# Kernel tuning notes

Measured on AMD Instinct MI355X. Metric: run time of the kernel, lower is better.

## Reference

```python
import jax, jax.numpy as jnp
import numpy as np

B, Q, P, K, E, H = 2, 2500, 2500, 2500, 256, 8
D = E // H
FF = 2 * E
EPS = 1e-5


def layernorm(x, g, b):
    mu = jnp.mean(x, axis=-1, keepdims=True)
    var = jnp.var(x, axis=-1, keepdims=True)
    return (x - mu) * jax.lax.rsqrt(var + EPS) * g + b


def mha(q_in, k_in, v_in, wq, wk, wv, scale):
    n, ql = q_in.shape[0], q_in.shape[1]
    q = (q_in @ wq).reshape(n, ql, H, D)
    k = (k_in @ wk).reshape(n, k_in.shape[1], H, D)
    v = (v_in @ wv).reshape(n, v_in.shape[1], H, D)
    scores = jnp.einsum('nqhd,nkhd->nhqk', q, k) / scale
    attn = jax.nn.softmax(scores, axis=-1)
    return jnp.einsum('nhqk,nkhd->nqhd', attn, v).reshape(n, ql, E)


def setup_inputs() -> dict:
    key = jax.random.key(0)
    ks = jax.random.split(key, 24)
    s = lambda i, shape, sc=0.02: jax.random.normal(ks[i], shape, dtype=jnp.float32) * sc
    return {
        'prev_seq': jax.random.normal(ks[0], (B, P, E), dtype=jnp.float32),
        'query': jax.random.normal(ks[1], (B, Q, E), dtype=jnp.float32),
        'img_ft': jax.random.normal(ks[2], (B, K, E), dtype=jnp.float32),
        't_wq': s(3, (E, E)), 't_wk': s(4, (E, E)), 't_wv': s(5, (E, E)),
        's_wq': s(6, (E, E)), 's_wk': s(7, (E, E)), 's_wv': s(8, (E, E)),
        's_wo': s(9, (E, E)), 's_bo': jnp.zeros((E,), jnp.float32),
        'n1_g': jnp.ones((E,), jnp.float32), 'n1_b': jnp.zeros((E,), jnp.float32),
        'n2_g': jnp.ones((E,), jnp.float32), 'n2_b': jnp.zeros((E,), jnp.float32),
        'n3_g': jnp.ones((E,), jnp.float32), 'n3_b': jnp.zeros((E,), jnp.float32),
        'ff_w1': s(10, (E, FF)), 'ff_b1': jnp.zeros((FF,), jnp.float32),
        'ff_w2': s(11, (FF, E)), 'ff_b2': jnp.zeros((E,), jnp.float32),
    }


def reference(prev_seq, query, img_ft, t_wq, t_wk, t_wv, s_wq, s_wk, s_wv,
              s_wo, s_bo, n1_g, n1_b, n2_g, n2_b, n3_g, n3_b,
              ff_w1, ff_b1, ff_w2, ff_b2):
    # Temporal self-attention: K/V from prev_seq, scale = sqrt(embed_size)
    attn = mha(query, prev_seq, prev_seq, t_wq, t_wk, t_wv, float(E) ** 0.5)
    x = layernorm(attn + query, n1_g, n1_b)
    # Spatial cross-attention: K/V from img_ft, scale = sqrt(head_dim), with fc_out
    cross = mha(x, img_ft, img_ft, s_wq, s_wk, s_wv, float(D) ** 0.5)
    cross = cross @ s_wo + s_bo
    x = layernorm(cross + x, n2_g, n2_b)
    # FFN: E -> 2E -> ReLU -> E
    ff = jax.nn.relu(x @ ff_w1 + ff_b1) @ ff_w2 + ff_b2
    return layernorm(ff + x, n3_g, n3_b)
```

## Files before the change

kernel.cpp:

```cpp
#include <hip/hip_runtime.h>
#include <hip/hip_bf16.h>
#include <stdint.h>


typedef __bf16 bf16_t;
typedef __bf16 bf16x8 __attribute__((ext_vector_type(8)));
typedef __bf16 bf16x4 __attribute__((ext_vector_type(4)));
typedef float  f32x4  __attribute__((ext_vector_type(4)));
typedef float  f32x16 __attribute__((ext_vector_type(16)));
typedef uint32_t u32;
typedef uint32_t u32x4 __attribute__((ext_vector_type(4)));

#define NB   2
#define SEQ  2500
#define EMB  256
#define NH   8
#define HD   32
#define MTOT (NB*SEQ)
#define KVSPLIT 5
#define SPLITLEN 500
#define NTILE 16

static __device__ __forceinline__ f32x4 mfma16(bf16x8 a, bf16x8 b, f32x4 c) {
  return __builtin_amdgcn_mfma_f32_16x16x32_bf16(a, b, c, 0, 0, 0);
}
static __device__ __forceinline__ f32x16 mfma32(bf16x8 a, bf16x8 b, f32x16 c) {
  return __builtin_amdgcn_mfma_f32_32x32x16_bf16(a, b, c, 0, 0, 0);
}
static __device__ __forceinline__ u32 pack2(float a, float b) {
  union { __bf16 h; unsigned short s; } x, y;
  x.h = (__bf16)a; y.h = (__bf16)b;
  return (u32)x.s | ((u32)y.s << 16);
}

__global__ __launch_bounds__(256) void prep_kernel(
    const float* s0, const float* s1, const float* s2, const float* s3,
    const float* s4, const float* s5, const float* s6, const float* s7,
    const float* s8, bf16_t* wt,
    const float* aq, const float* ap, const float* ai,
    bf16_t* dq, bf16_t* dp, bf16_t* di)
{
  int b = blockIdx.x;
  if (b < 176) {
    const float* src; int R, C, tl; size_t doff;
    if (b < 112) {
      int mi = b >> 4; tl = b & 15; R = 256; C = 256; doff = (size_t)mi * 65536;
      switch (mi) {
        case 0: src = s0; break; case 1: src = s1; break; case 2: src = s2; break;
        case 3: src = s3; break; case 4: src = s4; break; case 5: src = s5; break;
        default: src = s6;
      }
    } else if (b < 144) { tl = b - 112; R = 256; C = 512; doff = 458752; src = s7; }
    else                { tl = b - 144; R = 512; C = 256; doff = 589824; src = s8; }
    const int tpr = C >> 6;
    const int tr = tl / tpr, tc = tl % tpr;
    bf16_t* dst = wt + doff;
    #pragma unroll
    for (int i = 0; i < 16; ++i) {
      int lin = i * 256 + threadIdx.x;
      int lr = lin >> 6, lc = lin & 63;
      int rr = tr * 64 + lr, cc = tc * 64 + lc;
      dst[(size_t)cc * R + rr] = (__bf16)src[(size_t)rr * C + cc];
    }
    return;
  }
  int idx = b - 176;
  int t = idx / 313, r = idx % 313;
  const float* src = (t == 0) ? aq : (t == 1) ? ap : ai;
  bf16_t* dst = (t == 0) ? dq : (t == 1) ? dp : di;
  #pragma unroll
  for (int k = 0; k < 4; ++k) {
    int i = r * 1024 + k * 256 + threadIdx.x;
    if (i < 320000) {
      float4 v = ((const float4*)src)[i];
      bf16x4 o;
      o[0] = (__bf16)v.x; o[1] = (__bf16)v.y; o[2] = (__bf16)v.z; o[3] = (__bf16)v.w;
      ((bf16x4*)dst)[i] = o;
    }
  }
}

static __device__ __forceinline__ void gemm_body(
    const bf16_t* __restrict__ A, const bf16_t* __restrict__ Wt,
    const float* __restrict__ bias, bf16_t* __restrict__ Cout,
    int M, int N, int K, int relu, float cscale, int bx, int by)
{
  const int tid = threadIdx.x;
  const int lane = tid & 63, wid = tid >> 6;
  const int l15 = lane & 15, g = lane >> 4;
  const int mbase = bx * 64 + wid * 16;
  const int nbase = by * 64;

  int arow = mbase + l15; if (arow > M - 1) arow = M - 1;
  const bf16_t* ap = A + (size_t)arow * K + g * 8;
  const bf16_t* bp = Wt + (size_t)(nbase + l15) * K + g * 8;

  f32x4 acc[4];
  #pragma unroll
  for (int j = 0; j < 4; ++j) acc[j] = (f32x4){0.f,0.f,0.f,0.f};

  for (int kk = 0; kk < K; kk += 32) {
    bf16x8 a = *(const bf16x8*)(ap + kk);
    #pragma unroll
    for (int ct = 0; ct < 4; ++ct) {
      bf16x8 bfr = *(const bf16x8*)(bp + (size_t)ct * 16 * K + kk);
      acc[ct] = mfma16(a, bfr, acc[ct]);
    }
  }
  #pragma unroll
  for (int ct = 0; ct < 4; ++ct) {
    const int col = nbase + ct * 16 + l15;
    const float bv = bias ? bias[col] : 0.f;
    #pragma unroll
    for (int r = 0; r < 4; ++r) {
      const int row = mbase + g * 4 + r;
      if (row < M) {
        float v = acc[ct][r] * cscale + bv;
        if (relu) v = fmaxf(v, 0.f);
        Cout[(size_t)row * N + col] = (bf16_t)v;
      }
    }
  }
}

__global__ __launch_bounds__(256) void gemm_kernel(
    const bf16_t* __restrict__ A, const bf16_t* __restrict__ Wt,
    const float* __restrict__ bias, bf16_t* __restrict__ Cout,
    int M, int N, int K, int relu)
{
  gemm_body(A, Wt, bias, Cout, M, N, K, relu, 1.f, blockIdx.x, blockIdx.y);
}

__global__ __launch_bounds__(256) void proj3_kernel(
    const bf16_t* A0, const bf16_t* W0, bf16_t* C0,
    const bf16_t* A1, const bf16_t* W1, bf16_t* C1,
    const bf16_t* A2, const bf16_t* W2, bf16_t* C2, float qsc)
{
  const bf16_t* A = (blockIdx.z == 0) ? A0 : (blockIdx.z == 1) ? A1 : A2;
  const bf16_t* W = (blockIdx.z == 0) ? W0 : (blockIdx.z == 1) ? W1 : W2;
  bf16_t* C = (blockIdx.z == 0) ? C0 : (blockIdx.z == 1) ? C1 : C2;
  const float cs = (blockIdx.z == 0) ? qsc : 1.f;
  gemm_body(A, W, nullptr, C, MTOT, 256, 256, 0, cs, blockIdx.x, blockIdx.y);
}

__global__ __launch_bounds__(256, 4) void attn_part_kernel(
    const bf16_t* __restrict__ Qm, const bf16_t* __restrict__ Km,
    const bf16_t* __restrict__ Vm, bf16_t* __restrict__ Op,
    float* __restrict__ Lp)
{
  __shared__ bf16_t Vt[2][32][40];

  const int tid = threadIdx.x;
  const int lane = tid & 63, wid = tid >> 6;
  const int q32 = lane & 31, hi = lane >> 5;

  const int n = blockIdx.x;
  const int vid = (n & 7) * 200 + (n >> 3);
  const int grp = vid / 20;
  const int sub = vid - grp * 20;
  const int bh = grp / 5;
  const int split = grp - bh * 5;

  const size_t qoff = (size_t)(bh >> 3) * SEQ * EMB + (bh & 7) * HD;
  const int kv_begin = split * SPLITLEN;
  const int kv_end = kv_begin + SPLITLEN;

  const int qbase = sub * 128 + wid * 32;
  const int qr = min(qbase + q32, SEQ - 1);
  const bf16x8 qfa = *(const bf16x8*)(Qm + qoff + (size_t)qr * EMB + hi * 8);
  const bf16x8 qfb = *(const bf16x8*)(Qm + qoff + (size_t)qr * EMB + 16 + hi * 8);

  f32x16 acc = {};
  float lsum = 0.f;

  const int skv = tid >> 3;
  const int sd0 = (tid & 7) << 2;
  const int scc = (skv + ((sd0 >> 3) << 3)) & 31;

  const bf16_t* kp = Km + qoff + (size_t)(kv_begin + q32) * EMB + hi * 8;
  const bf16_t* vp = Vm + qoff + (size_t)(kv_begin + skv) * EMB + sd0;

  bf16x4 vreg = *(const bf16x4*)vp;
  vp += 32 * EMB;
  bf16x8 ka = *(const bf16x8*)kp;
  bf16x8 kb = *(const bf16x8*)(kp + 16);
  kp += 32 * EMB;

#define ATTN_TILE(T, MASKED, PREFETCH)                                         \
  {                                                                            \
    const int buf = (T) & 1;                                                   \
    _Pragma("unroll")                                                          \
    for (int j = 0; j < 4; ++j) Vt[buf][sd0 + j][scc] = vreg[j];               \
    bf16x4 vnext; bf16x8 kan, kbn;                                             \
    if (PREFETCH) {                                                            \
      vnext = *(const bf16x4*)vp;                                              \
      vp += 32 * EMB;                                                          \
      kan = *(const bf16x8*)kp;                                                \
      kbn = *(const bf16x8*)(kp + 16);                                         \
      kp += 32 * EMB;                                                          \
    }                                                                          \
    __syncthreads();                                                           \
    f32x16 s = {};                                                             \
    s = mfma32(ka, qfa, s);                                                    \
    s = mfma32(kb, qfb, s);                                                    \
    float p[16];                                                               \
    _Pragma("unroll")                                                          \
    for (int r = 0; r < 16; ++r) p[r] = __builtin_amdgcn_exp2f(s[r]);          \
    if (MASKED) {                                                              \
      const int kv0m = kv_begin + ((T) << 5);                                  \
      _Pragma("unroll")                                                        \
      for (int r = 0; r < 16; ++r) {                                           \
        const int kvg = kv0m + (r & 3) + ((r >> 2) << 3) + hi * 4;             \
        if (kvg >= kv_end) p[r] = 0.f;                                         \
      }                                                                        \
    }                                                                          \
    float ps = 0.f;                                                            \
    _Pragma("unroll")                                                          \
    for (int r = 0; r < 16; ++r) ps += p[r];                                   \
    lsum += ps;                                                                \
    u32 w0 = pack2(p[0], p[1]),   w1 = pack2(p[2], p[3]);                      \
    u32 w2 = pack2(p[4], p[5]),   w3 = pack2(p[6], p[7]);                      \
    u32 w4 = pack2(p[8], p[9]),   w5 = pack2(p[10], p[11]);                    \
    u32 w6 = pack2(p[12], p[13]), w7 = pack2(p[14], p[15]);                    \
    asm("v_permlane32_swap_b32 %0, %1" : "+v"(w0), "+v"(w2));                  \
    asm("v_permlane32_swap_b32 %0, %1" : "+v"(w1), "+v"(w3));                  \
    asm("v_permlane32_swap_b32 %0, %1" : "+v"(w4), "+v"(w6));                  \
    asm("v_permlane32_swap_b32 %0, %1" : "+v"(w5), "+v"(w7));                  \
    u32x4 f1, f2;                                                              \
    f1.x = w0; f1.y = w1; f1.z = w2; f1.w = w3;                                \
    f2.x = w4; f2.y = w5; f2.z = w6; f2.w = w7;                                \
    bf16x8 vf1 = *(const bf16x8*)&Vt[buf][q32][(((hi + (q32 >> 3)) & 3) << 3)];\
    bf16x8 vf2 = *(const bf16x8*)&Vt[buf][q32][(((2 + hi + (q32 >> 3)) & 3) << 3)]; \
    acc = mfma32(*(bf16x8*)&f1, vf1, acc);                                     \
    acc = mfma32(*(bf16x8*)&f2, vf2, acc);                                     \
    if (PREFETCH) { ka = kan; kb = kbn; vreg = vnext; }                        \
  }

  #pragma unroll 5
  for (int t = 0; t < NTILE - 1; ++t) ATTN_TILE(t, 0, 1)
  ATTN_TILE(NTILE - 1, 1, 0)
#undef ATTN_TILE

  lsum += __shfl_xor(lsum, 32);
  const size_t pbase = ((size_t)split * 16 + bh) * SEQ;
  #pragma unroll
  for (int r = 0; r < 16; ++r) {
    const int q = qbase + (r & 3) + ((r >> 2) << 3) + hi * 4;
    if (q < SEQ) Op[(pbase + q) * 32 + q32] = (bf16_t)acc[r];
  }
  if (lane < 32) {
    const int q = qbase + lane;
    if (q < SEQ) Lp[pbase + q] = lsum;
  }
}

__global__ __launch_bounds__(256) void merge_kernel(
    const bf16_t* __restrict__ Op, const float* __restrict__ Lp,
    const bf16_t* __restrict__ resid, const float* __restrict__ gw,
    const float* __restrict__ bw, bf16_t* __restrict__ out, int doLN)
{
  const int lane = threadIdx.x & 63, wid = threadIdx.x >> 6;
  const int row = blockIdx.x * 4 + wid;
  const int b = row / SEQ, q = row - b * SEQ;
  const int h = lane >> 3, dl = (lane & 7) * 4;
  const int bh = b * 8 + h;

  float L = 0.f;
  float acc[4] = {0.f, 0.f, 0.f, 0.f};
  #pragma unroll
  for (int s = 0; s < KVSPLIT; ++s) {
    const size_t pb = ((size_t)s * 16 + bh) * SEQ + q;
    L += Lp[pb];
    bf16x4 ov = *(const bf16x4*)(Op + pb * 32 + dl);
    #pragma unroll
    for (int j = 0; j < 4; ++j) acc[j] += (float)ov[j];
  }
  const float invL = 1.f / L;
  const size_t base = (size_t)row * EMB + lane * 4;
  if (!doLN) {
    bf16x4 ov;
    #pragma unroll
    for (int j = 0; j < 4; ++j) ov[j] = (__bf16)(acc[j] * invL);
    *(bf16x4*)(out + base) = ov;
    return;
  }
  bf16x4 rv = *(const bf16x4*)(resid + base);
  float x[4], s = 0.f, sq = 0.f;
  #pragma unroll
  for (int j = 0; j < 4; ++j) {
    x[j] = acc[j] * invL + (float)rv[j];
    s += x[j]; sq += x[j] * x[j];
  }
  #pragma unroll
  for (int m = 1; m < 64; m <<= 1) { s += __shfl_xor(s, m); sq += __shfl_xor(sq, m); }
  const float mean = s * (1.f / EMB);
  const float var = sq * (1.f / EMB) - mean * mean;
  const float rstd = rsqrtf(var + 1e-5f);
  float4 gv = *(const float4*)(gw + lane * 4);
  float4 bv = *(const float4*)(bw + lane * 4);
  bf16x4 ov;
  ov[0] = (__bf16)((x[0] - mean) * rstd * gv.x + bv.x);
  ov[1] = (__bf16)((x[1] - mean) * rstd * gv.y + bv.y);
  ov[2] = (__bf16)((x[2] - mean) * rstd * gv.z + bv.z);
  ov[3] = (__bf16)((x[3] - mean) * rstd * gv.w + bv.w);
  *(bf16x4*)(out + base) = ov;
}

__global__ __launch_bounds__(256) void ln_kernel(
    const bf16_t* __restrict__ A, const bf16_t* __restrict__ Bres,
    const float* __restrict__ gw, const float* __restrict__ bw,
    bf16_t* __restrict__ OutB, float* __restrict__ OutF, int M)
{
  const int lane = threadIdx.x & 63;
  const int wid = threadIdx.x >> 6;
  const int row = blockIdx.x * 4 + wid;
  if (row >= M) return;
  const size_t base = (size_t)row * EMB + lane * 4;
  bf16x4 av = *(const bf16x4*)(A + base);
  bf16x4 bv = *(const bf16x4*)(Bres + base);
  float x[4], s = 0.f, sq = 0.f;
  #pragma unroll
  for (int i = 0; i < 4; ++i) {
    x[i] = (float)av[i] + (float)bv[i];
    s += x[i]; sq += x[i] * x[i];
  }
  #pragma unroll
  for (int m = 1; m < 64; m <<= 1) { s += __shfl_xor(s, m); sq += __shfl_xor(sq, m); }
  const float mean = s * (1.f / EMB);
  const float var = sq * (1.f / EMB) - mean * mean;
  const float rstd = rsqrtf(var + 1e-5f);
  float4 gv = *(const float4*)(gw + lane * 4);
  float4 bev = *(const float4*)(bw + lane * 4);
  float y0 = (x[0] - mean) * rstd * gv.x + bev.x;
  float y1 = (x[1] - mean) * rstd * gv.y + bev.y;
  float y2 = (x[2] - mean) * rstd * gv.z + bev.z;
  float y3 = (x[3] - mean) * rstd * gv.w + bev.w;
  if (OutF) {
    float4 ov = {y0, y1, y2, y3};
    *(float4*)(OutF + base) = ov;
  } else {
    bf16x4 ov;
    ov[0] = (__bf16)y0; ov[1] = (__bf16)y1; ov[2] = (__bf16)y2; ov[3] = (__bf16)y3;
    *(bf16x4*)(OutB + base) = ov;
  }
}

extern "C" void kernel_launch(void* const* d_in, const int* in_sizes, int n_in,
                              void* d_out, int out_size, void* d_ws, size_t ws_size,
                              hipStream_t stream)
{
  (void)in_sizes; (void)n_in; (void)out_size; (void)ws_size;
  const float* prev  = (const float*)d_in[0];
  const float* query = (const float*)d_in[1];
  const float* img   = (const float*)d_in[2];
  const float* t_wq  = (const float*)d_in[3];
  const float* t_wk  = (const float*)d_in[4];
  const float* t_wv  = (const float*)d_in[5];
  const float* s_wq  = (const float*)d_in[6];
  const float* s_wk  = (const float*)d_in[7];
  const float* s_wv  = (const float*)d_in[8];
  const float* s_wo  = (const float*)d_in[9];
  const float* s_bo  = (const float*)d_in[10];
  const float* n1g = (const float*)d_in[11];
  const float* n1b = (const float*)d_in[12];
  const float* n2g = (const float*)d_in[13];
  const float* n2b = (const float*)d_in[14];
  const float* n3g = (const float*)d_in[15];
  const float* n3b = (const float*)d_in[16];
  const float* ffw1 = (const float*)d_in[17];
  const float* ffb1 = (const float*)d_in[18];
  const float* ffw2 = (const float*)d_in[19];
  const float* ffb2 = (const float*)d_in[20];

  bf16_t* ws   = (bf16_t*)d_ws;
  bf16_t* WT   = ws;
  bf16_t* WTF1 = ws + 458752;
  bf16_t* WTF2 = ws + 589824;
  bf16_t* qbf = ws + 720896;
  bf16_t* pbf = qbf + 1280000;
  bf16_t* ibf = pbf + 1280000;
  bf16_t* qb = ibf + 1280000;
  bf16_t* kb = qb + 1280000;
  bf16_t* vb = kb + 1280000;
  bf16_t* ab = vb + 1280000;
  bf16_t* x1 = ab + 1280000;
  bf16_t* cb = x1 + 1280000;
  bf16_t* x2 = cb + 1280000;
  bf16_t* hb = x2 + 1280000;
  bf16_t* fb = hb + 2560000;
  float* outp = (float*)d_out;
  bf16_t* Op = cb;
  float*  Lp = (float*)pbf;

  const float log2e = 1.4426950408889634f;
  const float qscT = log2e * (1.f / 16.f);
  const float qscS = log2e * 0.17677669529663687f;

  dim3 blk(256);
  prep_kernel<<<1115, blk, 0, stream>>>(t_wq, t_wk, t_wv, s_wq, s_wk, s_wv,
                                        s_wo, ffw1, ffw2, ws,
                                        query, prev, img, qbf, pbf, ibf);

  dim3 gP(79, 4, 3), gG256(79, 4), gG512(79, 8);
  proj3_kernel<<<gP, blk, 0, stream>>>(qbf, WT, qb,
                                       pbf, WT + 65536, kb,
                                       pbf, WT + 131072, vb, qscT);
  attn_part_kernel<<<1600, blk, 0, stream>>>(qb, kb, vb, Op, Lp);
  merge_kernel<<<1250, blk, 0, stream>>>(Op, Lp, qbf, n1g, n1b, x1, 1);
  proj3_kernel<<<gP, blk, 0, stream>>>(x1,  WT + 196608, qb,
                                       ibf, WT + 262144, kb,
                                       ibf, WT + 327680, vb, qscS);
  attn_part_kernel<<<1600, blk, 0, stream>>>(qb, kb, vb, Op, Lp);
  merge_kernel<<<1250, blk, 0, stream>>>(Op, Lp, nullptr, nullptr, nullptr, ab, 0);
  gemm_kernel<<<gG256, blk, 0, stream>>>(ab, WT + 393216, s_bo, cb, MTOT, 256, 256, 0);
  ln_kernel<<<1250, blk, 0, stream>>>(cb, x1, n2g, n2b, x2, nullptr, MTOT);
  gemm_kernel<<<gG512, blk, 0, stream>>>(x2, WTF1, ffb1, hb, MTOT, 512, 256, 1);
  gemm_kernel<<<gG256, blk, 0, stream>>>(hb, WTF2, ffb2, fb, MTOT, 256, 512, 0);
  ln_kernel<<<1250, blk, 0, stream>>>(fb, x2, n3g, n3b, nullptr, outp, MTOT);
}
```

Baseline: 197.2 us.

## Process attention KV tiles in pairs with dual accumulators for ILP

Restructures the split-KV attention inner loop to handle two 32-wide KV tiles per iteration, with separate score and output accumulators and interleaved MFMAs. This halves the number of __syncthreads barriers and exposes independent MFMA/exp chains to hide latency. The partial sums are also reduced with a tree instead of a serial chain. In exchange it doubles LDS for V tiles and raises register pressure, which could hurt occupancy under launch_bounds(256,4).

After: 199.5 us. Within noise of the previous version (+1.2%).

```diff
diff --git a/kernel.cpp b/kernel.cpp
--- a/kernel.cpp
+++ b/kernel.cpp
@@ -148,7 +148,7 @@
     const bf16_t* __restrict__ Vm, bf16_t* __restrict__ Op,
     float* __restrict__ Lp)
 {
-  __shared__ bf16_t Vt[2][32][40];
+  __shared__ bf16_t Vt[4][32][40];
 
   const int tid = threadIdx.x;
   const int lane = tid & 63, wid = tid >> 6;
@@ -170,7 +170,7 @@
   const bf16x8 qfa = *(const bf16x8*)(Qm + qoff + (size_t)qr * EMB + hi * 8);
   const bf16x8 qfb = *(const bf16x8*)(Qm + qoff + (size_t)qr * EMB + 16 + hi * 8);
 
-  f32x16 acc = {};
+  f32x16 accA = {}, accB = {};
   float lsum = 0.f;
 
   const int skv = tid >> 3;
@@ -180,73 +180,113 @@
   const bf16_t* kp = Km + qoff + (size_t)(kv_begin + q32) * EMB + hi * 8;
   const bf16_t* vp = Vm + qoff + (size_t)(kv_begin + skv) * EMB + sd0;
 
-  bf16x4 vreg = *(const bf16x4*)vp;
-  vp += 32 * EMB;
-  bf16x8 ka = *(const bf16x8*)kp;
-  bf16x8 kb = *(const bf16x8*)(kp + 16);
-  kp += 32 * EMB;
-
-#define ATTN_TILE(T, MASKED, PREFETCH)                                         \
+  bf16x4 vA = *(const bf16x4*)vp;
+  bf16x4 vB = *(const bf16x4*)(vp + 32 * EMB);
+  bf16x8 kaA = *(const bf16x8*)kp;
+  bf16x8 kbA = *(const bf16x8*)(kp + 16);
+  bf16x8 kaB = *(const bf16x8*)(kp + 32 * EMB);
+  bf16x8 kbB = *(const bf16x8*)(kp + 32 * EMB + 16);
+  kp += 64 * EMB;
+  vp += 64 * EMB;
+
+#define TREE16(dst, p)                                                         \
+    {                                                                          \
+      float t0 = p[0] + p[1],  t1 = p[2] + p[3];                               \
+      float t2 = p[4] + p[5],  t3 = p[6] + p[7];                               \
+      float t4 = p[8] + p[9],  t5 = p[10] + p[11];                             \
+      float t6 = p[12] + p[13], t7 = p[14] + p[15];                            \
+      float u0 = t0 + t1, u1 = t2 + t3, u2 = t4 + t5, u3 = t6 + t7;            \
+      dst = (u0 + u1) + (u2 + u3);                                             \
+    }
+
+#define SOFTPACK(p, f1, f2)                                                    \
+    {                                                                          \
+      u32 w0 = pack2(p[0], p[1]),   w1 = pack2(p[2], p[3]);                    \
+      u32 w2 = pack2(p[4], p[5]),   w3 = pack2(p[6], p[7]);                    \
+      u32 w4 = pack2(p[8], p[9]),   w5 = pack2(p[10], p[11]);                  \
+      u32 w6 = pack2(p[12], p[13]), w7 = pack2(p[14], p[15]);                  \
+      asm("v_permlane32_swap_b32 %0, %1" : "+v"(w0), "+v"(w2));                \
+      asm("v_permlane32_swap_b32 %0, %1" : "+v"(w1), "+v"(w3));                \
+      asm("v_permlane32_swap_b32 %0, %1" : "+v"(w4), "+v"(w6));                \
+      asm("v_permlane32_swap_b32 %0, %1" : "+v"(w5), "+v"(w7));                \
+      f1.x = w0; f1.y = w1; f1.z = w2; f1.w = w3;                              \
+      f2.x = w4; f2.y = w5; f2.z = w6; f2.w = w7;                              \
+    }
+
+#define ATTN_PAIR(P, MASKED, PREFETCH)                                         \
   {                                                                            \
-    const int buf = (T) & 1;                                                   \
+    const int bufA = ((P) & 1) << 1, bufB = bufA + 1;                          \
     _Pragma("unroll")                                                          \
-    for (int j = 0; j < 4; ++j) Vt[buf][sd0 + j][scc] = vreg[j];               \
-    bf16x4 vnext; bf16x8 kan, kbn;                                             \
+    for (int j = 0; j < 4; ++j) {                                              \
+      Vt[bufA][sd0 + j][scc] = vA[j];                                          \
+      Vt[bufB][sd0 + j][scc] = vB[j];                                          \
+    }                                                                          \
+    bf16x4 vAn, vBn; bf16x8 kaAn, kbAn, kaBn, kbBn;                            \
     if (PREFETCH) {                                                            \
-      vnext = *(const bf16x4*)vp;                                              \
-      vp += 32 * EMB;                                                          \
-      kan = *(const bf16x8*)kp;                                                \
-      kbn = *(const bf16x8*)(kp + 16);                                         \
-      kp += 32 * EMB;                                                          \
+      vAn = *(const bf16x4*)vp;                                                \
+      vBn = *(const bf16x4*)(vp + 32 * EMB);                                   \
+      kaAn = *(const bf16x8*)kp;                                               \
+      kbAn = *(const bf16x8*)(kp + 16);                                        \
+      kaBn = *(const bf16x8*)(kp + 32 * EMB);                                  \
+      kbBn = *(const bf16x8*)(kp + 32 * EMB + 16);                             \
+      kp += 64 * EMB; vp += 64 * EMB;                                          \
     }                                                                          \
     __syncthreads();                                                           \
-    f32x16 s = {};                                                             \
-    s = mfma32(ka, qfa, s);                                                    \
-    s = mfma32(kb, qfb, s);                                                    \
-    float p[16];                                                               \
+    f32x16 sA = {}, sB = {};                                                   \
+    sA = mfma32(kaA, qfa, sA);                                                 \
+    sB = mfma32(kaB, qfa, sB);                                                 \
+    sA = mfma32(kbA, qfb, sA);                                                 \
+    sB = mfma32(kbB, qfb, sB);                                                 \
+    float pA[16], pB[16];                                                      \
     _Pragma("unroll")                                                          \
-    for (int r = 0; r < 16; ++r) p[r] = __builtin_amdgcn_exp2f(s[r]);          \
+    for (int r = 0; r < 16; ++r) {                                             \
+      pA[r] = __builtin_amdgcn_exp2f(sA[r]);                                   \
+      pB[r] = __builtin_amdgcn_exp2f(sB[r]);                                   \
+    }                                                                          \
     if (MASKED) {                                                              \
-      const int kv0m = kv_begin + ((T) << 5);                                  \
+      const int kv0m = kv_begin + ((((P) << 1) + 1) << 5);                     \
       _Pragma("unroll")                                                        \
       for (int r = 0; r < 16; ++r) {                                           \
         const int kvg = kv0m + (r & 3) + ((r >> 2) << 3) + hi * 4;             \
-        if (kvg >= kv_end) p[r] = 0.f;                                         \
+        if (kvg >= kv_end) pB[r] = 0.f;                                        \
       }                                                                        \
     }                                                                          \
-    float ps = 0.f;                                                            \
-    _Pragma("unroll")                                                          \
-    for (int r = 0; r < 16; ++r) ps += p[r];                                   \
-    lsum += ps;                                                                \
-    u32 w0 = pack2(p[0], p[1]),   w1 = pack2(p[2], p[3]);                      \
-    u32 w2 = pack2(p[4], p[5]),   w3 = pack2(p[6], p[7]);                      \
-    u32 w4 = pack2(p[8], p[9]),   w5 = pack2(p[10], p[11]);                    \
-    u32 w6 = pack2(p[12], p[13]), w7 = pack2(p[14], p[15]);                    \
-    asm("v_permlane32_swap_b32 %0, %1" : "+v"(w0), "+v"(w2));                  \
-    asm("v_permlane32_swap_b32 %0, %1" : "+v"(w1), "+v"(w3));                  \
-    asm("v_permlane32_swap_b32 %0, %1" : "+v"(w4), "+v"(w6));                  \
-    asm("v_permlane32_swap_b32 %0, %1" : "+v"(w5), "+v"(w7));                  \
-    u32x4 f1, f2;                                                              \
-    f1.x = w0; f1.y = w1; f1.z = w2; f1.w = w3;                                \
-    f2.x = w4; f2.y = w5; f2.z = w6; f2.w = w7;                                \
-    bf16x8 vf1 = *(const bf16x8*)&Vt[buf][q32][(((hi + (q32 >> 3)) & 3) << 3)];\
-    bf16x8 vf2 = *(const bf16x8*)&Vt[buf][q32][(((2 + hi + (q32 >> 3)) & 3) << 3)]; \
-    acc = mfma32(*(bf16x8*)&f1, vf1, acc);                                     \
-    acc = mfma32(*(bf16x8*)&f2, vf2, acc);                                     \
-    if (PREFETCH) { ka = kan; kb = kbn; vreg = vnext; }                        \
-  }
-
-  #pragma unroll 5
-  for (int t = 0; t < NTILE - 1; ++t) ATTN_TILE(t, 0, 1)
-  ATTN_TILE(NTILE - 1, 1, 0)
-#undef ATTN_TILE
+    float psA, psB;                                                            \
+    TREE16(psA, pA)                                                            \
+    TREE16(psB, pB)                                                            \
+    lsum += psA + psB;                                                         \
+    u32x4 f1A, f2A, f1B, f2B;                                                  \
+    SOFTPACK(pA, f1A, f2A)                                                     \
+    SOFTPACK(pB, f1B, f2B)                                                     \
+    const int c1 = ((hi + (q32 >> 3)) & 3) << 3;                               \
+    const int c2 = ((2 + hi + (q32 >> 3)) & 3) << 3;                           \
+    bf16x8 vf1A = *(const bf16x8*)&Vt[bufA][q32][c1];                          \
+    bf16x8 vf2A = *(const bf16x8*)&Vt[bufA][q32][c2];                          \
+    bf16x8 vf1B = *(const bf16x8*)&Vt[bufB][q32][c1];                          \
+    bf16x8 vf2B = *(const bf16x8*)&Vt[bufB][q32][c2];                          \
+    accA = mfma32(*(bf16x8*)&f1A, vf1A, accA);                                 \
+    accB = mfma32(*(bf16x8*)&f1B, vf1B, accB);                                 \
+    accA = mfma32(*(bf16x8*)&f2A, vf2A, accA);                                 \
+    accB = mfma32(*(bf16x8*)&f2B, vf2B, accB);                                 \
+    if (PREFETCH) {                                                            \
+      kaA = kaAn; kbA = kbAn; kaB = kaBn; kbB = kbBn;                          \
+      vA = vAn; vB = vBn;                                                      \
+    }                                                                          \
+  }
+
+  #pragma unroll
+  for (int P = 0; P < 7; ++P) ATTN_PAIR(P, 0, 1)
+  ATTN_PAIR(7, 1, 0)
+#undef ATTN_PAIR
+#undef SOFTPACK
+#undef TREE16
 
   lsum += __shfl_xor(lsum, 32);
   const size_t pbase = ((size_t)split * 16 + bh) * SEQ;
   #pragma unroll
   for (int r = 0; r < 16; ++r) {
     const int q = qbase + (r & 3) + ((r >> 2) << 3) + hi * 4;
-    if (q < SEQ) Op[(pbase + q) * 32 + q32] = (bf16_t)acc[r];
+    if (q < SEQ) Op[(pbase + q) * 32 + q32] = (bf16_t)(accA[r] + accB[r]);
   }
   if (lane < 32) {
     const int q = qbase + lane;
```
